# Kernel optimization log

Measured on AMD Instinct MI355X. Metric: run time of the kernel, lower is better.

Reference implementation:

```python
import jax, jax.numpy as jnp
import numpy as np

N_NODES = 50000
N_EDGES = 600000
D_IN = 128
D_H = 128


def _sage_layer(h, src, dst, deg_inv, W_self, W_neigh, b):
    # gather src features along edges, sum into dst, then mean-normalize
    msum = jax.ops.segment_sum(h[src], dst, num_segments=N_NODES)  # [N, d]
    h_neigh = msum * deg_inv[:, None]
    return h @ W_self + h_neigh @ W_neigh + b


def setup_inputs() -> dict:
    key = jax.random.key(0)
    ks = jax.random.split(key, 10)
    inp = {
        'g_features': jax.random.normal(ks[0], (N_NODES, D_IN), dtype=jnp.float32),
        'src': jax.random.randint(ks[1], (N_EDGES,), 0, N_NODES, dtype=jnp.int32),
        'dst': jax.random.randint(ks[2], (N_EDGES,), 0, N_NODES, dtype=jnp.int32),
    }
    scale_in = 1.0 / np.sqrt(D_IN)
    scale_h = 1.0 / np.sqrt(D_H)
    inp['W_self1'] = jax.random.normal(ks[3], (D_IN, D_H), dtype=jnp.float32) * scale_in
    inp['W_neigh1'] = jax.random.normal(ks[4], (D_IN, D_H), dtype=jnp.float32) * scale_in
    inp['b1'] = jnp.zeros((D_H,), dtype=jnp.float32)
    inp['W_self2'] = jax.random.normal(ks[5], (D_H, D_H), dtype=jnp.float32) * scale_h
    inp['W_neigh2'] = jax.random.normal(ks[6], (D_H, D_H), dtype=jnp.float32) * scale_h
    inp['b2'] = jnp.zeros((D_H,), dtype=jnp.float32)
    inp['W_self3'] = jax.random.normal(ks[7], (D_H, D_H), dtype=jnp.float32) * scale_h
    inp['W_neigh3'] = jax.random.normal(ks[8], (D_H, D_H), dtype=jnp.float32) * scale_h
    inp['b3'] = jnp.zeros((D_H,), dtype=jnp.float32)
    return inp


def reference(g_features, src, dst, W_self1, W_neigh1, b1, W_self2, W_neigh2, b2, W_self3, W_neigh3, b3):
    # in-degree per dst node, clamped to >= 1 (DGL SAGEConv mean)
    deg = jax.ops.segment_sum(jnp.ones_like(dst, dtype=g_features.dtype), dst, num_segments=N_NODES)
    deg_inv = 1.0 / jnp.maximum(deg, 1.0)

    h = _sage_layer(g_features, src, dst, deg_inv, W_self1, W_neigh1, b1)
    h = jax.nn.relu(h)
    h = _sage_layer(h, src, dst, deg_inv, W_self2, W_neigh2, b2)
    h = jax.nn.relu(h)
    h = _sage_layer(h, src, dst, deg_inv, W_self3, W_neigh3, b3)
    return h
```

## Files before the change

kernel.cpp:

```cpp
#include <hip/hip_runtime.h>
#include <hip/hip_bf16.h>

#define N_NODES 50000
#define N_EDGES 600000
#define D 128
#define BM 32

typedef __bf16 bf16x8 __attribute__((ext_vector_type(8)));
typedef float f32x4 __attribute__((ext_vector_type(4)));

__device__ __forceinline__ float bits2f(unsigned int u) {
    union { unsigned int i; float f; } t; t.i = u; return t.f;
}
__device__ __forceinline__ unsigned short f2bf(float x) {
    unsigned int u = __builtin_bit_cast(unsigned int, x);
    unsigned int r = (u + 0x7fff + ((u >> 16) & 1)) >> 16;
    return (unsigned short)r;
}

#define PREP_CVT_BLOCKS 6250
#define PREP_HIST_BLOCKS 2344
#define PREP_W_BLOCKS 384
__global__ void prep_kernel(const float* __restrict__ feat, unsigned short* __restrict__ g_bf,
                            const int* __restrict__ dst, int* __restrict__ deg,
                            const float* w0, const float* w1, const float* w2,
                            const float* w3, const float* w4, const float* w5,
                            unsigned short* __restrict__ WT) {
    int b = blockIdx.x;
    if (b < PREP_CVT_BLOCKS) {
        int i = b * 256 + threadIdx.x;
        if (i < N_NODES * D / 4) {
            float4 v = *(const float4*)(feat + (size_t)i * 4);
            ushort4 o;
            o.x = f2bf(v.x); o.y = f2bf(v.y); o.z = f2bf(v.z); o.w = f2bf(v.w);
            *(ushort4*)(g_bf + (size_t)i * 4) = o;
        }
    } else if (b < PREP_CVT_BLOCKS + PREP_HIST_BLOCKS) {
        int i = (b - PREP_CVT_BLOCKS) * 256 + threadIdx.x;
        if (i < N_EDGES) atomicAdd(&deg[dst[i]], 1);
    } else {
        int j = (b - PREP_CVT_BLOCKS - PREP_HIST_BLOCKS) * 256 + threadIdx.x;
        int m = j >> 14;
        int e = j & 16383;
        const float* src = m == 0 ? w0 : m == 1 ? w1 : m == 2 ? w2 : m == 3 ? w3 : m == 4 ? w4 : w5;
        int n = e >> 7, k = e & 127;
        WT[m * 16384 + n * 128 + k] = f2bf(src[k * 128 + n]);
    }
}

__global__ void scan1_kernel(const int* __restrict__ deg, int* __restrict__ partial,
                             int* __restrict__ blk_sums) {
    __shared__ int ws[16];
    int i = blockIdx.x * 1024 + threadIdx.x;
    int x = (i < N_NODES) ? deg[i] : 0;
    int lane = threadIdx.x & 63, wid = threadIdx.x >> 6;
    int v = x;
    #pragma unroll
    for (int off = 1; off < 64; off <<= 1) {
        int t = __shfl_up(v, off);
        if (lane >= off) v += t;
    }
    if (lane == 63) ws[wid] = v;
    __syncthreads();
    if (threadIdx.x == 0) {
        int c = 0;
        #pragma unroll
        for (int j = 0; j < 16; ++j) { int t = ws[j]; ws[j] = c; c += t; }
        blk_sums[blockIdx.x] = c;
    }
    __syncthreads();
    if (i < N_NODES) partial[i] = v - x + ws[wid];
}

__global__ void scan2_kernel(int* __restrict__ blk_sums, int nb) {
    int lane = threadIdx.x;
    int v = (lane < nb) ? blk_sums[lane] : 0;
    int x = v;
    #pragma unroll
    for (int off = 1; off < 64; off <<= 1) {
        int t = __shfl_up(v, off);
        if (lane >= off) v += t;
    }
    if (lane < nb) blk_sums[lane] = v - x;
}

__global__ void scan3_kernel(const int* __restrict__ partial, const int* __restrict__ blk_sums,
                             const int* __restrict__ deg, int* __restrict__ row_start,
                             int* __restrict__ cursor, float* __restrict__ deg_inv) {
    int i = blockIdx.x * 256 + threadIdx.x;
    if (i < N_NODES) {
        int rs = partial[i] + blk_sums[i >> 10];
        row_start[i] = rs;
        cursor[i] = rs;
        deg_inv[i] = 1.0f / fmaxf((float)deg[i], 1.0f);
    }
    if (i == 0) row_start[N_NODES] = N_EDGES;
}

__global__ void fill_kernel(const int* __restrict__ src, const int* __restrict__ dst,
                            int* __restrict__ cursor, int* __restrict__ esrc, int n) {
    int i = blockIdx.x * blockDim.x + threadIdx.x;
    if (i < n) {
        int p = atomicAdd(&cursor[dst[i]], 1);
        esrc[p] = src[i];
    }
}

__device__ __forceinline__ void acc_add(float* a, uint4 v) {
    unsigned int w[4] = {v.x, v.y, v.z, v.w};
    #pragma unroll
    for (int j = 0; j < 4; ++j) {
        a[2*j]   += bits2f(w[j] << 16);
        a[2*j+1] += bits2f(w[j] & 0xffff0000u);
    }
}

__global__ __launch_bounds__(256) void layer_kernel(
        const unsigned short* __restrict__ h, const int* __restrict__ row_start,
        const int* __restrict__ esrc, const float* __restrict__ deg_inv,
        const unsigned short* __restrict__ WsT, const unsigned short* __restrict__ WnT,
        const float* __restrict__ bias, void* __restrict__ outp,
        int do_relu, int store_f32) {
    __shared__ char lds[BM * 256 * 2];
    char* Ah = lds;
    char* Am = lds + BM * 256;
    int tid = threadIdx.x;
    int l = tid & 63, w = tid >> 6;
    int row0 = blockIdx.x * BM;

    bf16x8 bfrag[2][2][4];
    {
        size_t off = (size_t)(w * 32 + (l & 15)) * D + ((l >> 4) * 8);
        const unsigned short* Wp0 = WsT + off;
        const unsigned short* Wp1 = WnT + off;
        #pragma unroll
        for (int nt = 0; nt < 2; ++nt)
            #pragma unroll
            for (int ks = 0; ks < 4; ++ks) {
                bfrag[0][nt][ks] = *(const bf16x8*)(Wp0 + nt * 16 * D + ks * 32);
                bfrag[1][nt][ks] = *(const bf16x8*)(Wp1 + nt * 16 * D + ks * 32);
            }
    }

    #pragma unroll
    for (int i = 0; i < 2; ++i) {
        int c = tid + i * 256;
        int r = c >> 4, ch = c & 15;
        int gr = row0 + r; if (gr >= N_NODES) gr = N_NODES - 1;
        uint4 v = *(const uint4*)(h + (size_t)gr * D + ch * 8);
        *(uint4*)(Ah + r * 256 + ((ch << 4) ^ ((r & 7) << 4))) = v;
    }

    {
        int gi = tid >> 4, l16 = tid & 15;
        const unsigned short* hl = h + l16 * 8;
        #pragma unroll
        for (int nn = 0; nn < 2; ++nn) {
            int r = gi * 2 + nn;
            int node = row0 + r;
            float acc[8] = {0, 0, 0, 0, 0, 0, 0, 0};
            float di = 0.f;
            if (node < N_NODES) {
                int s = row_start[node], e = row_start[node + 1];
                int k = s;
                for (; k + 4 <= e; k += 4) {
                    int i0 = esrc[k], i1 = esrc[k + 1], i2 = esrc[k + 2], i3 = esrc[k + 3];
                    uint4 v0 = *(const uint4*)(hl + (size_t)i0 * D);
                    uint4 v1 = *(const uint4*)(hl + (size_t)i1 * D);
                    uint4 v2 = *(const uint4*)(hl + (size_t)i2 * D);
                    uint4 v3 = *(const uint4*)(hl + (size_t)i3 * D);
                    acc_add(acc, v0); acc_add(acc, v1); acc_add(acc, v2); acc_add(acc, v3);
                }
                for (; k < e; ++k) {
                    uint4 v = *(const uint4*)(hl + (size_t)esrc[k] * D);
                    acc_add(acc, v);
                }
                di = deg_inv[node];
            }
            unsigned short o[8];
            #pragma unroll
            for (int j = 0; j < 8; ++j) o[j] = f2bf(acc[j] * di);
            *(uint4*)(Am + r * 256 + ((l16 << 4) ^ ((r & 7) << 4))) = *(uint4*)o;
        }
    }
    __syncthreads();

    f32x4 acc[2][2];
    #pragma unroll
    for (int mt = 0; mt < 2; ++mt)
        #pragma unroll
        for (int nt = 0; nt < 2; ++nt)
            acc[mt][nt] = (f32x4)0.0f;

    #pragma unroll
    for (int ph = 0; ph < 2; ++ph) {
        char* Ab = ph ? Am : Ah;
        #pragma unroll
        for (int ks = 0; ks < 4; ++ks) {
            int kb = ks * 64 + ((l >> 4) << 4);
            bf16x8 a[2];
            #pragma unroll
            for (int mt = 0; mt < 2; ++mt) {
                int r = mt * 16 + (l & 15);
                a[mt] = *(const bf16x8*)(Ab + r * 256 + (kb ^ ((r & 7) << 4)));
            }
            #pragma unroll
            for (int mt = 0; mt < 2; ++mt)
                #pragma unroll
                for (int nt = 0; nt < 2; ++nt)
                    acc[mt][nt] = __builtin_amdgcn_mfma_f32_16x16x32_bf16(a[mt], bfrag[ph][nt][ks], acc[mt][nt], 0, 0, 0);
        }
    }

    #pragma unroll
    for (int nt = 0; nt < 2; ++nt) {
        int col = w * 32 + nt * 16 + (l & 15);
        float bv = bias[col];
        #pragma unroll
        for (int mt = 0; mt < 2; ++mt) {
            #pragma unroll
            for (int r = 0; r < 4; ++r) {
                int grow = row0 + mt * 16 + ((l >> 4) << 2) + r;
                if (grow < N_NODES) {
                    float v = acc[mt][nt][r] + bv;
                    if (do_relu) v = fmaxf(v, 0.f);
                    if (store_f32) ((float*)outp)[(size_t)grow * D + col] = v;
                    else ((unsigned short*)outp)[(size_t)grow * D + col] = f2bf(v);
                }
            }
        }
    }
}

static inline size_t align_up(size_t x, size_t a) { return (x + a - 1) & ~(a - 1); }

extern "C" void kernel_launch(void* const* d_in, const int* in_sizes, int n_in,
                              void* d_out, int out_size, void* d_ws, size_t ws_size,
                              hipStream_t stream) {
    const float* g_feat = (const float*)d_in[0];
    const int* src = (const int*)d_in[1];
    const int* dst = (const int*)d_in[2];
    const float* Ws1 = (const float*)d_in[3];
    const float* Wn1 = (const float*)d_in[4];
    const float* b1  = (const float*)d_in[5];
    const float* Ws2 = (const float*)d_in[6];
    const float* Wn2 = (const float*)d_in[7];
    const float* b2  = (const float*)d_in[8];
    const float* Ws3 = (const float*)d_in[9];
    const float* Wn3 = (const float*)d_in[10];
    const float* b3  = (const float*)d_in[11];
    float* out = (float*)d_out;

    char* ws = (char*)d_ws;
    int* deg        = (int*)ws;            ws += align_up(N_NODES * 4, 256);
    int* row_start  = (int*)ws;            ws += align_up((N_NODES + 1) * 4, 256);
    int* cursor     = (int*)ws;            ws += align_up(N_NODES * 4, 256);
    float* deg_inv  = (float*)ws;          ws += align_up(N_NODES * 4, 256);
    int* partial    = (int*)ws;            ws += align_up(N_NODES * 4, 256);
    int* blk_sums   = (int*)ws;            ws += align_up(64 * 4, 256);
    int* esrc       = (int*)ws;            ws += align_up(N_EDGES * 4, 256);
    unsigned short* g_bf = (unsigned short*)ws;  ws += align_up((size_t)N_NODES * D * 2, 256);
    unsigned short* WT   = (unsigned short*)ws;  ws += align_up(6 * 128 * 128 * 2, 256);
    unsigned short* bufA = (unsigned short*)ws;  ws += align_up((size_t)N_NODES * D * 2, 256);
    unsigned short* bufB = (unsigned short*)ws;  ws += align_up((size_t)N_NODES * D * 2, 256);

    hipMemsetAsync(deg, 0, N_NODES * 4, stream);
    prep_kernel<<<PREP_CVT_BLOCKS + PREP_HIST_BLOCKS + PREP_W_BLOCKS, 256, 0, stream>>>(
        g_feat, g_bf, dst, deg, Ws1, Wn1, Ws2, Wn2, Ws3, Wn3, WT);
    int nb = (N_NODES + 1023) / 1024;
    scan1_kernel<<<nb, 1024, 0, stream>>>(deg, partial, blk_sums);
    scan2_kernel<<<1, 64, 0, stream>>>(blk_sums, nb);
    scan3_kernel<<<(N_NODES + 255) / 256, 256, 0, stream>>>(partial, blk_sums, deg, row_start, cursor, deg_inv);
    fill_kernel<<<(N_EDGES + 255) / 256, 256, 0, stream>>>(src, dst, cursor, esrc, N_EDGES);

    dim3 grid((N_NODES + BM - 1) / BM);
    const unsigned short *WsT1 = WT, *WnT1 = WT + 16384, *WsT2 = WT + 2*16384,
                         *WnT2 = WT + 3*16384, *WsT3 = WT + 4*16384, *WnT3 = WT + 5*16384;

    layer_kernel<<<grid, 256, 0, stream>>>(g_bf, row_start, esrc, deg_inv, WsT1, WnT1, b1, bufA, 1, 0);
    layer_kernel<<<grid, 256, 0, stream>>>(bufA, row_start, esrc, deg_inv, WsT2, WnT2, b2, bufB, 1, 0);
    layer_kernel<<<grid, 256, 0, stream>>>(bufB, row_start, esrc, deg_inv, WsT3, WnT3, b3, out, 0, 1);
}
```

Measured before the change: 320.6 us.

## Single-block scan, dynamic per-node gather scheduling, direct self-term fragment loads

Replaces the three-kernel degree scan with one 1024-thread block that scans 52 nodes per thread and writes row_start, cursor and deg_inv directly. This removes two launches and the intermediate partial buffers. In the layer kernel, 16-lane groups now take nodes dynamically through an LDS atomic counter, which balances irregular degrees, and the gather unroll is widened to 8. Self-feature A fragments are loaded straight from global memory into registers instead of staged through LDS, which halves LDS use. The neighbour weight fragments are loaded after the gather, which cuts register pressure during that phase.

```diff
diff --git a/kernel.cpp b/kernel.cpp
--- a/kernel.cpp
+++ b/kernel.cpp
@@ -48,53 +48,72 @@
     }
 }
 
-__global__ void scan1_kernel(const int* __restrict__ deg, int* __restrict__ partial,
-                             int* __restrict__ blk_sums) {
+__global__ __launch_bounds__(1024) void scan_all_kernel(const int* __restrict__ deg,
+        int* __restrict__ row_start, int* __restrict__ cursor, float* __restrict__ deg_inv) {
     __shared__ int ws[16];
-    int i = blockIdx.x * 1024 + threadIdx.x;
-    int x = (i < N_NODES) ? deg[i] : 0;
-    int lane = threadIdx.x & 63, wid = threadIdx.x >> 6;
-    int v = x;
+    int t = threadIdx.x;
+    int base = t * 52;
+    uint4 d[13];
+    #pragma unroll
+    for (int j = 0; j < 13; ++j) {
+        int idx = base + j * 4;
+        if (idx + 4 <= N_NODES) {
+            d[j] = *(const uint4*)(deg + idx);
+        } else {
+            unsigned a = (idx < N_NODES) ? (unsigned)deg[idx] : 0u;
+            unsigned bb = (idx + 1 < N_NODES) ? (unsigned)deg[idx + 1] : 0u;
+            unsigned c = (idx + 2 < N_NODES) ? (unsigned)deg[idx + 2] : 0u;
+            unsigned dd = (idx + 3 < N_NODES) ? (unsigned)deg[idx + 3] : 0u;
+            d[j] = make_uint4(a, bb, c, dd);
+        }
+    }
+    int s = 0;
+    #pragma unroll
+    for (int j = 0; j < 13; ++j) s += (int)(d[j].x + d[j].y + d[j].z + d[j].w);
+    int lane = t & 63, wid = t >> 6;
+    int v = s;
     #pragma unroll
     for (int off = 1; off < 64; off <<= 1) {
-        int t = __shfl_up(v, off);
-        if (lane >= off) v += t;
+        int tmp = __shfl_up(v, off);
+        if (lane >= off) v += tmp;
     }
     if (lane == 63) ws[wid] = v;
     __syncthreads();
-    if (threadIdx.x == 0) {
+    if (t == 0) {
         int c = 0;
         #pragma unroll
-        for (int j = 0; j < 16; ++j) { int t = ws[j]; ws[j] = c; c += t; }
-        blk_sums[blockIdx.x] = c;
+        for (int j = 0; j < 16; ++j) { int x = ws[j]; ws[j] = c; c += x; }
     }
     __syncthreads();
-    if (i < N_NODES) partial[i] = v - x + ws[wid];
-}
-
-__global__ void scan2_kernel(int* __restrict__ blk_sums, int nb) {
-    int lane = threadIdx.x;
-    int v = (lane < nb) ? blk_sums[lane] : 0;
-    int x = v;
-    #pragma unroll
-    for (int off = 1; off < 64; off <<= 1) {
-        int t = __shfl_up(v, off);
-        if (lane >= off) v += t;
-    }
-    if (lane < nb) blk_sums[lane] = v - x;
-}
-
-__global__ void scan3_kernel(const int* __restrict__ partial, const int* __restrict__ blk_sums,
-                             const int* __restrict__ deg, int* __restrict__ row_start,
-                             int* __restrict__ cursor, float* __restrict__ deg_inv) {
-    int i = blockIdx.x * 256 + threadIdx.x;
-    if (i < N_NODES) {
-        int rs = partial[i] + blk_sums[i >> 10];
-        row_start[i] = rs;
-        cursor[i] = rs;
-        deg_inv[i] = 1.0f / fmaxf((float)deg[i], 1.0f);
-    }
-    if (i == 0) row_start[N_NODES] = N_EDGES;
+    int run = v - s + ws[wid];
+    #pragma unroll
+    for (int j = 0; j < 13; ++j) {
+        int vals[4] = {(int)d[j].x, (int)d[j].y, (int)d[j].z, (int)d[j].w};
+        int rs[4];
+        #pragma unroll
+        for (int q = 0; q < 4; ++q) { rs[q] = run; run += vals[q]; }
+        int idx = base + j * 4;
+        if (idx + 4 <= N_NODES) {
+            *(int4*)(row_start + idx) = make_int4(rs[0], rs[1], rs[2], rs[3]);
+            *(int4*)(cursor + idx) = make_int4(rs[0], rs[1], rs[2], rs[3]);
+            float4 di;
+            di.x = 1.0f / fmaxf((float)vals[0], 1.0f);
+            di.y = 1.0f / fmaxf((float)vals[1], 1.0f);
+            di.z = 1.0f / fmaxf((float)vals[2], 1.0f);
+            di.w = 1.0f / fmaxf((float)vals[3], 1.0f);
+            *(float4*)(deg_inv + idx) = di;
+        } else {
+            #pragma unroll
+            for (int q = 0; q < 4; ++q) {
+                if (idx + q < N_NODES) {
+                    row_start[idx + q] = rs[q];
+                    cursor[idx + q] = rs[q];
+                    deg_inv[idx + q] = 1.0f / fmaxf((float)vals[q], 1.0f);
+                }
+            }
+        }
+    }
+    if (t == 1023) row_start[N_NODES] = N_EDGES;
 }
 
 __global__ void fill_kernel(const int* __restrict__ src, const int* __restrict__ dst,
@@ -107,11 +126,11 @@
 }
 
 __device__ __forceinline__ void acc_add(float* a, uint4 v) {
-    unsigned int w[4] = {v.x, v.y, v.z, v.w};
+    unsigned int wv[4] = {v.x, v.y, v.z, v.w};
     #pragma unroll
     for (int j = 0; j < 4; ++j) {
-        a[2*j]   += bits2f(w[j] << 16);
-        a[2*j+1] += bits2f(w[j] & 0xffff0000u);
+        a[2*j]   += bits2f(wv[j] << 16);
+        a[2*j+1] += bits2f(wv[j] & 0xffff0000u);
     }
 }
 
@@ -121,67 +140,87 @@
         const unsigned short* __restrict__ WsT, const unsigned short* __restrict__ WnT,
         const float* __restrict__ bias, void* __restrict__ outp,
         int do_relu, int store_f32) {
-    __shared__ char lds[BM * 256 * 2];
-    char* Ah = lds;
-    char* Am = lds + BM * 256;
+    __shared__ char Am[BM * 256];
+    __shared__ int rs_s[BM + 1];
+    __shared__ float dinv_s[BM];
+    __shared__ int ctr_s;
     int tid = threadIdx.x;
     int l = tid & 63, w = tid >> 6;
     int row0 = blockIdx.x * BM;
 
-    bf16x8 bfrag[2][2][4];
+    bf16x8 b0[2][4];
     {
         size_t off = (size_t)(w * 32 + (l & 15)) * D + ((l >> 4) * 8);
-        const unsigned short* Wp0 = WsT + off;
-        const unsigned short* Wp1 = WnT + off;
         #pragma unroll
         for (int nt = 0; nt < 2; ++nt)
             #pragma unroll
-            for (int ks = 0; ks < 4; ++ks) {
-                bfrag[0][nt][ks] = *(const bf16x8*)(Wp0 + nt * 16 * D + ks * 32);
-                bfrag[1][nt][ks] = *(const bf16x8*)(Wp1 + nt * 16 * D + ks * 32);
-            }
-    }
-
-    #pragma unroll
-    for (int i = 0; i < 2; ++i) {
-        int c = tid + i * 256;
-        int r = c >> 4, ch = c & 15;
-        int gr = row0 + r; if (gr >= N_NODES) gr = N_NODES - 1;
-        uint4 v = *(const uint4*)(h + (size_t)gr * D + ch * 8);
-        *(uint4*)(Ah + r * 256 + ((ch << 4) ^ ((r & 7) << 4))) = v;
-    }
-
+            for (int ks = 0; ks < 4; ++ks)
+                b0[nt][ks] = *(const bf16x8*)(WsT + off + nt * 16 * D + ks * 32);
+    }
+    if (tid <= BM) {
+        int node = row0 + tid;
+        rs_s[tid] = row_start[node <= N_NODES ? node : N_NODES];
+    }
+    if (tid < BM) {
+        int node = row0 + tid;
+        dinv_s[tid] = (node < N_NODES) ? deg_inv[node] : 0.f;
+    }
+    if (tid == 0) ctr_s = 0;
+    __syncthreads();
+
+    int l16 = tid & 15;
+    const unsigned short* hl = h + l16 * 8;
+    for (;;) {
+        int n;
+        if (l16 == 0) n = atomicAdd(&ctr_s, 1);
+        n = __shfl(n, l & 48);
+        if (n >= BM) break;
+        float acc[8] = {0, 0, 0, 0, 0, 0, 0, 0};
+        int s = rs_s[n], e = rs_s[n + 1];
+        int k = s;
+        for (; k + 8 <= e; k += 8) {
+            int i0 = esrc[k],     i1 = esrc[k + 1], i2 = esrc[k + 2], i3 = esrc[k + 3];
+            int i4 = esrc[k + 4], i5 = esrc[k + 5], i6 = esrc[k + 6], i7 = esrc[k + 7];
+            uint4 v0 = *(const uint4*)(hl + (size_t)i0 * D);
+            uint4 v1 = *(const uint4*)(hl + (size_t)i1 * D);
+            uint4 v2 = *(const uint4*)(hl + (size_t)i2 * D);
+            uint4 v3 = *(const uint4*)(hl + (size_t)i3 * D);
+            uint4 v4 = *(const uint4*)(hl + (size_t)i4 * D);
+            uint4 v5 = *(const uint4*)(hl + (size_t)i5 * D);
+            uint4 v6 = *(const uint4*)(hl + (size_t)i6 * D);
+            uint4 v7 = *(const uint4*)(hl + (size_t)i7 * D);
+            acc_add(acc, v0); acc_add(acc, v1); acc_add(acc, v2); acc_add(acc, v3);
+            acc_add(acc, v4); acc_add(acc, v5); acc_add(acc, v6); acc_add(acc, v7);
+        }
+        for (; k < e; ++k) {
+            uint4 v = *(const uint4*)(hl + (size_t)esrc[k] * D);
+            acc_add(acc, v);
+        }
+        float sc = dinv_s[n];
+        unsigned short o[8];
+        #pragma unroll
+        for (int j = 0; j < 8; ++j) o[j] = f2bf(acc[j] * sc);
+        *(uint4*)(Am + n * 256 + ((l16 << 4) ^ ((n & 7) << 4))) = *(uint4*)o;
+    }
+
+    bf16x8 a0[2][4];
+    #pragma unroll
+    for (int mt = 0; mt < 2; ++mt) {
+        int r = row0 + mt * 16 + (l & 15);
+        if (r >= N_NODES) r = N_NODES - 1;
+        const unsigned short* hp = h + (size_t)r * D + ((l >> 4) * 8);
+        #pragma unroll
+        for (int ks = 0; ks < 4; ++ks)
+            a0[mt][ks] = *(const bf16x8*)(hp + ks * 32);
+    }
+    bf16x8 b1[2][4];
     {
-        int gi = tid >> 4, l16 = tid & 15;
-        const unsigned short* hl = h + l16 * 8;
-        #pragma unroll
-        for (int nn = 0; nn < 2; ++nn) {
-            int r = gi * 2 + nn;
-            int node = row0 + r;
-            float acc[8] = {0, 0, 0, 0, 0, 0, 0, 0};
-            float di = 0.f;
-            if (node < N_NODES) {
-                int s = row_start[node], e = row_start[node + 1];
-                int k = s;
-                for (; k + 4 <= e; k += 4) {
-                    int i0 = esrc[k], i1 = esrc[k + 1], i2 = esrc[k + 2], i3 = esrc[k + 3];
-                    uint4 v0 = *(const uint4*)(hl + (size_t)i0 * D);
-                    uint4 v1 = *(const uint4*)(hl + (size_t)i1 * D);
-                    uint4 v2 = *(const uint4*)(hl + (size_t)i2 * D);
-                    uint4 v3 = *(const uint4*)(hl + (size_t)i3 * D);
-                    acc_add(acc, v0); acc_add(acc, v1); acc_add(acc, v2); acc_add(acc, v3);
-                }
-                for (; k < e; ++k) {
-                    uint4 v = *(const uint4*)(hl + (size_t)esrc[k] * D);
-                    acc_add(acc, v);
-                }
-                di = deg_inv[node];
-            }
-            unsigned short o[8];
-            #pragma unroll
-            for (int j = 0; j < 8; ++j) o[j] = f2bf(acc[j] * di);
-            *(uint4*)(Am + r * 256 + ((l16 << 4) ^ ((r & 7) << 4))) = *(uint4*)o;
-        }
+        size_t off = (size_t)(w * 32 + (l & 15)) * D + ((l >> 4) * 8);
+        #pragma unroll
+        for (int nt = 0; nt < 2; ++nt)
+            #pragma unroll
+            for (int ks = 0; ks < 4; ++ks)
+                b1[nt][ks] = *(const bf16x8*)(WnT + off + nt * 16 * D + ks * 32);
     }
     __syncthreads();
 
@@ -193,23 +232,27 @@
             acc[mt][nt] = (f32x4)0.0f;
 
     #pragma unroll
-    for (int ph = 0; ph < 2; ++ph) {
-        char* Ab = ph ? Am : Ah;
-        #pragma unroll
-        for (int ks = 0; ks < 4; ++ks) {
-            int kb = ks * 64 + ((l >> 4) << 4);
-            bf16x8 a[2];
-            #pragma unroll
-            for (int mt = 0; mt < 2; ++mt) {
-                int r = mt * 16 + (l & 15);
-                a[mt] = *(const bf16x8*)(Ab + r * 256 + (kb ^ ((r & 7) << 4)));
-            }
-            #pragma unroll
-            for (int mt = 0; mt < 2; ++mt)
-                #pragma unroll
-                for (int nt = 0; nt < 2; ++nt)
-                    acc[mt][nt] = __builtin_amdgcn_mfma_f32_16x16x32_bf16(a[mt], bfrag[ph][nt][ks], acc[mt][nt], 0, 0, 0);
-        }
+    for (int ks = 0; ks < 4; ++ks)
+        #pragma unroll
+        for (int mt = 0; mt < 2; ++mt)
+            #pragma unroll
+            for (int nt = 0; nt < 2; ++nt)
+                acc[mt][nt] = __builtin_amdgcn_mfma_f32_16x16x32_bf16(a0[mt][ks], b0[nt][ks], acc[mt][nt], 0, 0, 0);
+
+    #pragma unroll
+    for (int ks = 0; ks < 4; ++ks) {
+        int kb = ks * 64 + ((l >> 4) << 4);
+        bf16x8 a[2];
+        #pragma unroll
+        for (int mt = 0; mt < 2; ++mt) {
+            int r = mt * 16 + (l & 15);
+            a[mt] = *(const bf16x8*)(Am + r * 256 + (kb ^ ((r & 7) << 4)));
+        }
+        #pragma unroll
+        for (int mt = 0; mt < 2; ++mt)
+            #pragma unroll
+            for (int nt = 0; nt < 2; ++nt)
+                acc[mt][nt] = __builtin_amdgcn_mfma_f32_16x16x32_bf16(a[mt], b1[nt][ks], acc[mt][nt], 0, 0, 0);
     }
 
     #pragma unroll
@@ -256,8 +299,6 @@
     int* row_start  = (int*)ws;            ws += align_up((N_NODES + 1) * 4, 256);
     int* cursor     = (int*)ws;            ws += align_up(N_NODES * 4, 256);
     float* deg_inv  = (float*)ws;          ws += align_up(N_NODES * 4, 256);
-    int* partial    = (int*)ws;            ws += align_up(N_NODES * 4, 256);
-    int* blk_sums   = (int*)ws;            ws += align_up(64 * 4, 256);
     int* esrc       = (int*)ws;            ws += align_up(N_EDGES * 4, 256);
     unsigned short* g_bf = (unsigned short*)ws;  ws += align_up((size_t)N_NODES * D * 2, 256);
     unsigned short* WT   = (unsigned short*)ws;  ws += align_up(6 * 128 * 128 * 2, 256);
@@ -267,10 +308,7 @@
     hipMemsetAsync(deg, 0, N_NODES * 4, stream);
     prep_kernel<<<PREP_CVT_BLOCKS + PREP_HIST_BLOCKS + PREP_W_BLOCKS, 256, 0, stream>>>(
         g_feat, g_bf, dst, deg, Ws1, Wn1, Ws2, Wn2, Ws3, Wn3, WT);
-    int nb = (N_NODES + 1023) / 1024;
-    scan1_kernel<<<nb, 1024, 0, stream>>>(deg, partial, blk_sums);
-    scan2_kernel<<<1, 64, 0, stream>>>(blk_sums, nb);
-    scan3_kernel<<<(N_NODES + 255) / 256, 256, 0, stream>>>(partial, blk_sums, deg, row_start, cursor, deg_inv);
+    scan_all_kernel<<<1, 1024, 0, stream>>>(deg, row_start, cursor, deg_inv);
     fill_kernel<<<(N_EDGES + 255) / 256, 256, 0, stream>>>(src, dst, cursor, esrc, N_EDGES);
 
     dim3 grid((N_NODES + BM - 1) / BM);
```

New measurement: 365.5 us. 1.14x slower.
